# Optimization experiments

Hardware: AMD Instinct MI355X
Metric: run time of the kernel (lower is better)

The kernel has to match this reference:

```python
import jax, jax.numpy as jnp
import numpy as np

S, B, H = 2048, 2, 1024
NH = 16
HD = H // NH
EPS = 1e-5


def _ln(z, w, b):
    m = jnp.mean(z, axis=-1, keepdims=True)
    v = jnp.mean(jnp.square(z - m), axis=-1, keepdims=True)
    return (z - m) * jax.lax.rsqrt(v + EPS) * w + b


def setup_inputs() -> dict:
    key = jax.random.key(0)
    ks = jax.random.split(key, 8)
    std = 0.02
    return {
        "x": jax.random.normal(ks[0], (S, B, H), dtype=jnp.float32),
        "ln1_w": jnp.ones((H,), jnp.float32),
        "ln1_b": jnp.zeros((H,), jnp.float32),
        "w_qkv": jax.random.normal(ks[1], (3 * H, H), jnp.float32) * std,
        "b_qkv": jnp.zeros((3 * H,), jnp.float32),
        "w_proj": jax.random.normal(ks[2], (H, H), jnp.float32) * std,
        "b_proj": jnp.zeros((H,), jnp.float32),
        "ln2_w": jnp.ones((H,), jnp.float32),
        "ln2_b": jnp.zeros((H,), jnp.float32),
        "w_fc1": jax.random.normal(ks[3], (4 * H, H), jnp.float32) * std,
        "b_fc1": jnp.zeros((4 * H,), jnp.float32),
        "w_fc2": jax.random.normal(ks[4], (H, 4 * H), jnp.float32) * std,
        "b_fc2": jnp.zeros((H,), jnp.float32),
    }


def reference(x, ln1_w, ln1_b, w_qkv, b_qkv, w_proj, b_proj,
              ln2_w, ln2_b, w_fc1, b_fc1, w_fc2, b_fc2):
    s, b, h = x.shape
    # --- LayerNormLinear: LN then fused QKV projection ---
    residual = x
    qkv = _ln(x, ln1_w, ln1_b) @ w_qkv.T + b_qkv            # [S, B, 3H]
    # per-head interleaved packing: [S, B, NH, 3*HD] then split on last dim
    qkv = qkv.reshape(s, b, NH, 3 * HD).transpose(1, 2, 0, 3)  # [B, NH, S, 3HD]
    q, k, v = jnp.split(qkv, 3, axis=3)                      # each [B, NH, S, HD]
    # --- naive causal attention with full SxS scores ---
    scores = jnp.einsum("bhsd,bhtd->bhst", q, k) * (HD ** -0.5)
    causal = jnp.triu(jnp.ones((s, s), dtype=bool), k=1)
    scores = jnp.where(causal, -jnp.inf, scores)
    attn = jax.nn.softmax(scores, axis=-1)                   # [B, NH, S, S]
    out = jnp.einsum("bhst,bhtd->bhsd", attn, v)             # [B, NH, S, HD]
    out = out.transpose(0, 2, 1, 3).reshape(b, s, h).transpose(1, 0, 2)  # [S, B, H]
    out = out @ w_proj.T + b_proj
    x = residual + out
    # --- LayerNormMLP: LN -> fc1 -> gelu(tanh) -> fc2, residual ---
    residual = x
    hmid = jax.nn.gelu(_ln(x, ln2_w, ln2_b) @ w_fc1.T + b_fc1, approximate=True)
    x = residual + (hmid @ w_fc2.T + b_fc2)
    return x
```

## Files before the change

### kernel.cpp

```cpp
#include <hip/hip_runtime.h>
#include <math.h>

#define S_LEN 2048
#define B_SZ 2
#define NHEAD 16
#define HDIM 64
#define H_DIM 1024
#define M_ROWS (S_LEN * B_SZ)
#define LN_EPS 1e-5f
#define KSTR 72
#define SCL 0.18033688011112042f

typedef __attribute__((ext_vector_type(4))) float f32x4;
typedef __attribute__((ext_vector_type(8))) short short8;
typedef __attribute__((ext_vector_type(8))) unsigned short u16x8;
typedef __attribute__((ext_vector_type(4))) unsigned short u16x4;
typedef __attribute__((ext_vector_type(2))) unsigned short u16x2;

typedef __attribute__((address_space(3))) unsigned int lds_u32;
typedef const __attribute__((address_space(1))) unsigned int glb_u32;

#define ASM_VMCNT(N) asm volatile("s_waitcnt vmcnt(" #N ")" ::: "memory")

__device__ __forceinline__ float bf2f(unsigned short u) {
    return __uint_as_float(((unsigned int)u) << 16);
}
__device__ __forceinline__ unsigned short f2bf(float f) {
    unsigned int u = __float_as_uint(f);
    return (unsigned short)((u + 0x7fffu + ((u >> 16) & 1u)) >> 16);
}

__global__ __launch_bounds__(256) void cast_all(const float* __restrict__ wqkv,
                                                const float* __restrict__ wproj,
                                                const float* __restrict__ wfc1,
                                                const float* __restrict__ wfc2,
                                                unsigned short* __restrict__ oqkv,
                                                unsigned short* __restrict__ oproj,
                                                unsigned short* __restrict__ ofc1,
                                                unsigned short* __restrict__ ofc2) {
    const int i = blockIdx.x * 256 + threadIdx.x;
    const float* src; unsigned short* dst; int off;
    if (i < 786432)       { src = wqkv;  dst = oqkv;  off = i; }
    else if (i < 1048576) { src = wproj; dst = oproj; off = i - 786432; }
    else if (i < 2097152) { src = wfc1;  dst = ofc1;  off = i - 1048576; }
    else                  { src = wfc2;  dst = ofc2;  off = i - 2097152; }
    f32x4 v = ((const f32x4*)src)[off];
    u16x4 o;
    o.x = f2bf(v.x); o.y = f2bf(v.y); o.z = f2bf(v.z); o.w = f2bf(v.w);
    ((u16x4*)dst)[off] = o;
}

__global__ __launch_bounds__(256) void ln_bf16(const float* __restrict__ x,
                                               const float* __restrict__ w,
                                               const float* __restrict__ b,
                                               unsigned short* __restrict__ y) {
    const int m = blockIdx.x;
    const int tid = threadIdx.x;
    const float* row = x + (size_t)m * H_DIM;

    float4 v = ((const float4*)row)[tid];
    float s  = v.x + v.y + v.z + v.w;
    float ss = v.x * v.x + v.y * v.y + v.z * v.z + v.w * v.w;

    __shared__ float rs[4], rss[4], stats[2];
    const int wave = tid >> 6, lane = tid & 63;
    for (int off = 32; off; off >>= 1) {
        s  += __shfl_down(s, off);
        ss += __shfl_down(ss, off);
    }
    if (lane == 0) { rs[wave] = s; rss[wave] = ss; }
    __syncthreads();
    if (tid == 0) {
        float S = rs[0] + rs[1] + rs[2] + rs[3];
        float SS = rss[0] + rss[1] + rss[2] + rss[3];
        float mean = S * (1.0f / H_DIM);
        float var = SS * (1.0f / H_DIM) - mean * mean;
        stats[0] = mean;
        stats[1] = rsqrtf(var + LN_EPS);
    }
    __syncthreads();
    const float mean = stats[0], inv = stats[1];
    float4 wv = ((const float4*)w)[tid];
    float4 bv = ((const float4*)b)[tid];
    u16x4 o;
    o.x = f2bf((v.x - mean) * inv * wv.x + bv.x);
    o.y = f2bf((v.y - mean) * inv * wv.y + bv.y);
    o.z = f2bf((v.z - mean) * inv * wv.z + bv.z);
    o.w = f2bf((v.w - mean) * inv * wv.w + bv.w);
    ((u16x4*)(y + (size_t)m * H_DIM))[tid] = o;
}

template <int EPI, bool BF_OUT, int TN>
__global__ __launch_bounds__(256) void gemm_mfma(const unsigned short* __restrict__ A,
                                                 const unsigned short* __restrict__ B,
                                                 const float* __restrict__ bias,
                                                 const float* __restrict__ resid,
                                                 void* __restrict__ Cout,
                                                 int M, int N, int K) {
    constexpr int NJ  = TN / 32;
    constexpr int ANI = 4;
    constexpr int BNI = TN / 32;
    constexpr int NBUF = (TN == 128) ? 2 : 3;
    __shared__ __attribute__((aligned(16))) unsigned short As[NBUF][128 * 64];
    __shared__ __attribute__((aligned(16))) unsigned short Bs[NBUF][TN * 64];

    const int tid = threadIdx.x;
    const int wid = tid >> 6;
    const int ln  = tid & 63;
    const int quad = ln >> 4;
    const int mr   = ln & 15;
    const int wm = (wid >> 1) * 64;
    const int wn = (wid & 1) * (TN / 2);

    const int mb = M >> 7;
    const int stripe = mb >> 3;
    const int xcd = blockIdx.x & 7;
    const int local = blockIdx.x >> 3;
    const int m0 = (xcd * stripe + (local % stripe)) << 7;
    const int n0 = (local / stripe) * TN;

    const int lr = ln >> 3, lc = ln & 7;
    const size_t Kb = (size_t)K * 2;
    const char* gA = (const char*)A + (size_t)(m0 + wid * 32 + lr) * Kb
                     + (size_t)((lc << 4) ^ (lr << 4));
    const int bwr = (TN == 128) ? wid * 32 : wid * 16;
    const char* gB = (const char*)B + (size_t)(n0 + bwr + lr) * Kb
                     + (size_t)((lc << 4) ^ (lr << 4));

    auto stage = [&](int kt, int buf) {
        const char* pa = gA + (size_t)kt * 128;
        unsigned int* la = (unsigned int*)&As[buf][0] + wid * (ANI * 256);
#pragma unroll
        for (int i = 0; i < ANI; i++)
            __builtin_amdgcn_global_load_lds((glb_u32*)(pa + (size_t)i * 8 * Kb),
                                             (lds_u32*)(la + i * 256), 16, 0, 0);
        const char* pb = gB + (size_t)kt * 128;
        unsigned int* lb = (unsigned int*)&Bs[buf][0] + wid * (BNI * 256);
#pragma unroll
        for (int i = 0; i < BNI; i++)
            __builtin_amdgcn_global_load_lds((glb_u32*)(pb + (size_t)i * 8 * Kb),
                                             (lds_u32*)(lb + i * 256), 16, 0, 0);
    };

    const f32x4 zero = {0.f, 0.f, 0.f, 0.f};
    f32x4 acc[4][NJ];
#pragma unroll
    for (int i = 0; i < 4; i++)
#pragma unroll
        for (int j = 0; j < NJ; j++) acc[i][j] = zero;

    const int swz = (mr & 7) << 3;
    auto compute = [&](const unsigned short* As_, const unsigned short* Bs_) {
#pragma unroll
        for (int h = 0; h < 2; h++) {
            short8 af[4], bfr[NJ];
#pragma unroll
            for (int i = 0; i < 4; i++)
                af[i] = *(const short8*)(As_ + (wm + i * 16 + mr) * 64
                                             + ((h * 32 + quad * 8) ^ swz));
#pragma unroll
            for (int j = 0; j < NJ; j++)
                bfr[j] = *(const short8*)(Bs_ + (wn + j * 16 + mr) * 64
                                              + ((h * 32 + quad * 8) ^ swz));
#pragma unroll
            for (int i = 0; i < 4; i++)
#pragma unroll
                for (int j = 0; j < NJ; j++)
                    acc[i][j] = __builtin_amdgcn_mfma_f32_16x16x32_bf16(bfr[j], af[i], acc[i][j], 0, 0, 0);
        }
    };

    const int nt = K >> 6;
    stage(0, 0);
    stage(1, 1);
    if (NBUF == 3) stage(2, 2);

    int cb = 0;
    for (int kt = 0; kt < nt; kt++) {
        if (NBUF == 3) {
            if (kt + 2 < nt)      ASM_VMCNT(12);
            else if (kt + 1 < nt) ASM_VMCNT(6);
            else                  ASM_VMCNT(0);
        } else {
            if (kt + 1 < nt)      ASM_VMCNT(8);
            else                  ASM_VMCNT(0);
        }
        __builtin_amdgcn_s_barrier();
        __builtin_amdgcn_sched_barrier(0);
        compute(&As[cb][0], &Bs[cb][0]);
        __builtin_amdgcn_sched_barrier(0);
        __builtin_amdgcn_s_barrier();
        if (kt + NBUF < nt) stage(kt + NBUF, cb);
        cb = (cb + 1 == NBUF) ? 0 : cb + 1;
    }

    f32x4 bias4[NJ];
#pragma unroll
    for (int j = 0; j < NJ; j++)
        bias4[j] = *(const f32x4*)(bias + n0 + wn + j * 16 + quad * 4);

#pragma unroll
    for (int i = 0; i < 4; i++) {
        const int m = m0 + wm + i * 16 + mr;
#pragma unroll
        for (int j = 0; j < NJ; j++) {
            const int nb = n0 + wn + j * 16 + quad * 4;
            f32x4 v = acc[i][j] + bias4[j];
            if (EPI == 1) v += *(const f32x4*)(resid + (size_t)m * N + nb);
            if (EPI == 2) {
#pragma unroll
                for (int r = 0; r < 4; r++) {
                    const float t = v[r];
                    const float u = t + 0.044715f * t * t * t;
                    const float e = exp2f(2.3022112f * u);
                    v[r] = t - t / (e + 1.0f);
                }
            }
            if (BF_OUT) {
                u16x4 pk;
                pk.x = f2bf(v.x); pk.y = f2bf(v.y); pk.z = f2bf(v.z); pk.w = f2bf(v.w);
                *(u16x4*)((unsigned short*)Cout + (size_t)m * N + nb) = pk;
            } else {
                *(f32x4*)((float*)Cout + (size_t)m * N + nb) = v;
            }
        }
    }
}

__global__ __launch_bounds__(256) void attn_mfma(const unsigned short* __restrict__ qkv,
                                                 unsigned short* __restrict__ out) {
    __shared__ __attribute__((aligned(16))) unsigned short Ks[64 * KSTR];
    __shared__ __attribute__((aligned(16))) unsigned short Vs[64 * KSTR];
    __shared__ __attribute__((aligned(16))) unsigned short Ps[64 * KSTR];

    const int tid = threadIdx.x;
    const int wid = tid >> 6;
    const int ln  = tid & 63;
    const int quad = ln >> 4;
    const int mr   = ln & 15;

    const int id = blockIdx.x;
    const int local = id >> 3;
    const int bh = (id & 7) * 4 + (local >> 4);
    const int pa = local & 15;
    const int b  = bh >> 4;
    const int nh = bh & 15;
    const size_t chan = (size_t)nh * 192;

    const int ksr = tid >> 2, ksc = tid & 3;
    const int vt0 = (tid & 31) * 2, vd0 = (tid >> 5) * 8;

    u16x8 kp0, kp1, vp0, vp1;

#pragma unroll
    for (int half = 0; half < 2; half++) {
        const int qt = half ? (31 - pa) : pa;
        const int qb = qt * 64;

        short8 qf0, qf1;
        {
            const int qrow = qb + wid * 16 + mr;
            const unsigned short* gq = qkv + ((size_t)(qrow * 2 + b)) * 3072 + chan + quad * 8;
            qf0 = *(const short8*)gq;
            qf1 = *(const short8*)(gq + 32);
        }

        const f32x4 zero = {0.f, 0.f, 0.f, 0.f};
        f32x4 o[4];
        float ps = 0.f;
#pragma unroll
        for (int d = 0; d < 4; d++) o[d] = zero;

        {
            const unsigned short* gk = qkv + ((size_t)(ksr * 2 + b)) * 3072 + chan + 64 + ksc * 16;
            kp0 = *(const u16x8*)gk;
            kp1 = *(const u16x8*)(gk + 8);
            const unsigned short* gv = qkv + ((size_t)(vt0 * 2 + b)) * 3072 + chan + 128 + vd0;
            vp0 = *(const u16x8*)gv;
            vp1 = *(const u16x8*)(gv + 6144);
        }

        for (int kt = 0; kt <= qt; kt++) {
            __syncthreads();
            *(u16x8*)(Ks + ksr * KSTR + ksc * 16) = kp0;
            *(u16x8*)(Ks + ksr * KSTR + ksc * 16 + 8) = kp1;
#pragma unroll
            for (int j = 0; j < 8; j++) {
                u16x2 pr; pr.x = vp0[j]; pr.y = vp1[j];
                *(u16x2*)(Vs + (vd0 + j) * KSTR + vt0) = pr;
            }
            if (kt < qt) {
                const int nb = (kt + 1) * 64;
                const unsigned short* gk =
                    qkv + ((size_t)((nb + ksr) * 2 + b)) * 3072 + chan + 64 + ksc * 16;
                kp0 = *(const u16x8*)gk;
                kp1 = *(const u16x8*)(gk + 8);
                const unsigned short* gv =
                    qkv + ((size_t)((nb + vt0) * 2 + b)) * 3072 + chan + 128 + vd0;
                vp0 = *(const u16x8*)gv;
                vp1 = *(const u16x8*)(gv + 6144);
            }
            __syncthreads();

            f32x4 sacc[4];
#pragma unroll
            for (int n = 0; n < 4; n++) {
                sacc[n] = zero;
                const unsigned short* kb = Ks + (n * 16 + mr) * KSTR + quad * 8;
                short8 kfr0 = *(const short8*)kb;
                short8 kfr1 = *(const short8*)(kb + 32);
                sacc[n] = __builtin_amdgcn_mfma_f32_16x16x32_bf16(kfr0, qf0, sacc[n], 0, 0, 0);
                sacc[n] = __builtin_amdgcn_mfma_f32_16x16x32_bf16(kfr1, qf1, sacc[n], 0, 0, 0);
            }
            if (kt == qt) {
#pragma unroll
                for (int n = 0; n < 4; n++)
#pragma unroll
                    for (int r = 0; r < 4; r++)
                        if (n * 16 + quad * 4 + r > wid * 16 + mr) sacc[n][r] = -3.0e38f;
            }

            unsigned short* prow = Ps + (wid * 16 + mr) * KSTR + quad * 4;
#pragma unroll
            for (int n = 0; n < 4; n++) {
                u16x4 pk;
#pragma unroll
                for (int r = 0; r < 4; r++) {
                    const float p = exp2f(fminf(sacc[n][r] * SCL, 80.f));
                    ps += p;
                    pk[r] = (unsigned short)(__float_as_uint(p) >> 16);
                }
                *(u16x4*)(prow + n * 16) = pk;
            }

            {
                const unsigned short* pb = Ps + (wid * 16 + mr) * KSTR + quad * 8;
                short8 pa0 = *(const short8*)pb;
                short8 pa1 = *(const short8*)(pb + 32);
#pragma unroll
                for (int d = 0; d < 4; d++) {
                    const unsigned short* vb = Vs + (d * 16 + mr) * KSTR + quad * 8;
                    short8 vf0 = *(const short8*)vb;
                    short8 vf1 = *(const short8*)(vb + 32);
                    o[d] = __builtin_amdgcn_mfma_f32_16x16x32_bf16(vf0, pa0, o[d], 0, 0, 0);
                    o[d] = __builtin_amdgcn_mfma_f32_16x16x32_bf16(vf1, pa1, o[d], 0, 0, 0);
                }
            }
        }

        ps += __shfl_xor(ps, 16);
        ps += __shfl_xor(ps, 32);
        const float inv = 1.0f / ps;
        const int qrow = qb + wid * 16 + mr;
        unsigned short* po = out + ((size_t)(qrow * 2 + b)) * H_DIM + nh * HDIM;
#pragma unroll
        for (int d = 0; d < 4; d++) {
            u16x4 pk;
#pragma unroll
            for (int r = 0; r < 4; r++) pk[r] = f2bf(o[d][r] * inv);
            *(u16x4*)(po + d * 16 + quad * 4) = pk;
        }
    }
}

extern "C" void kernel_launch(void* const* d_in, const int* in_sizes, int n_in,
                              void* d_out, int out_size, void* d_ws, size_t ws_size,
                              hipStream_t stream) {
    const float* x      = (const float*)d_in[0];
    const float* ln1_w  = (const float*)d_in[1];
    const float* ln1_b  = (const float*)d_in[2];
    const float* w_qkv  = (const float*)d_in[3];
    const float* b_qkv  = (const float*)d_in[4];
    const float* w_proj = (const float*)d_in[5];
    const float* b_proj = (const float*)d_in[6];
    const float* ln2_w  = (const float*)d_in[7];
    const float* ln2_b  = (const float*)d_in[8];
    const float* w_fc1  = (const float*)d_in[9];
    const float* b_fc1  = (const float*)d_in[10];
    const float* w_fc2  = (const float*)d_in[11];
    const float* b_fc2  = (const float*)d_in[12];
    float* out = (float*)d_out;

    char* ws = (char*)d_ws;
    unsigned short* wqkv_bf  = (unsigned short*)(ws);
    unsigned short* wproj_bf = (unsigned short*)(ws + ((size_t)6 << 20));
    unsigned short* wfc1_bf  = (unsigned short*)(ws + ((size_t)8 << 20));
    unsigned short* wfc2_bf  = (unsigned short*)(ws + ((size_t)16 << 20));
    unsigned short* ln_buf   = (unsigned short*)(ws + ((size_t)24 << 20));
    unsigned short* qkv_bf   = (unsigned short*)(ws + ((size_t)32 << 20));
    unsigned short* attn_bf  = (unsigned short*)(ws + ((size_t)56 << 20));
    unsigned short* fc1_bf   = (unsigned short*)(ws + ((size_t)32 << 20));

    cast_all<<<12288, 256, 0, stream>>>(w_qkv, w_proj, w_fc1, w_fc2,
                                        wqkv_bf, wproj_bf, wfc1_bf, wfc2_bf);

    ln_bf16<<<M_ROWS, 256, 0, stream>>>(x, ln1_w, ln1_b, ln_buf);
    gemm_mfma<0, true, 128><<<768, 256, 0, stream>>>(
        ln_buf, wqkv_bf, b_qkv, nullptr, qkv_bf, M_ROWS, 3072, 1024);
    attn_mfma<<<512, 256, 0, stream>>>(qkv_bf, attn_bf);
    gemm_mfma<1, false, 64><<<512, 256, 0, stream>>>(
        attn_bf, wproj_bf, b_proj, x, out, M_ROWS, 1024, 1024);
    ln_bf16<<<M_ROWS, 256, 0, stream>>>(out, ln2_w, ln2_b, ln_buf);
    gemm_mfma<2, true, 128><<<1024, 256, 0, stream>>>(
        ln_buf, wfc1_bf, b_fc1, nullptr, fc1_bf, M_ROWS, 4096, 1024);
    gemm_mfma<1, false, 64><<<512, 256, 0, stream>>>(
        fc1_bf, wfc2_bf, b_fc2, out, out, M_ROWS, 1024, 4096);
}
```

Measured before the change: 339.2 us.

## Add 256x256-tile 8-wave GEMM with ping-pong LDS pipeline for QKV and FC1

Adds a new GEMM kernel with 512 threads and 256x256 output tiles. It uses a 4-slot LDS ring filled by direct global-to-LDS loads, XOR swizzling, and split A/B staging interleaved with MFMA phases under barriers and setprio. The QKV and FC1 projections use this kernel instead of the 128-tile one, aiming for more operand reuse and better overlap of loads with MFMA work. The trade-off is fewer blocks (192 and 256, near one per CU) and high register pressure from 32 accumulators per thread, so tail effects and occupancy are at risk.

```diff
diff --git a/kernel.cpp b/kernel.cpp
--- a/kernel.cpp
+++ b/kernel.cpp
@@ -21,6 +21,7 @@
 typedef const __attribute__((address_space(1))) unsigned int glb_u32;
 
 #define ASM_VMCNT(N) asm volatile("s_waitcnt vmcnt(" #N ")" ::: "memory")
+#define ASM_LGKM0()  asm volatile("s_waitcnt lgkmcnt(0)" ::: "memory")
 
 __device__ __forceinline__ float bf2f(unsigned short u) {
     return __uint_as_float(((unsigned int)u) << 16);
@@ -227,6 +228,148 @@
     }
 }
 
+template <int EPI, bool BF_OUT>
+__global__ __launch_bounds__(512, 1) void gemm_8p(const unsigned short* __restrict__ A,
+                                                  const unsigned short* __restrict__ B,
+                                                  const float* __restrict__ bias,
+                                                  const float* __restrict__ resid,
+                                                  void* __restrict__ Cout,
+                                                  int M, int N, int K) {
+    constexpr int SLOT = 256 * 32 * 2;
+    __shared__ __attribute__((aligned(16))) unsigned short Ls[4 * SLOT];
+
+    const int tid = threadIdx.x;
+    const int wid = tid >> 6;
+    const int ln  = tid & 63;
+    const int quad = ln >> 4;
+    const int mr   = ln & 15;
+    const int wr = wid >> 2;
+    const int wc = wid & 3;
+
+    const int nm = M >> 8;
+    const int stripe = nm >> 3;
+    const int xcd = blockIdx.x & 7;
+    const int local = blockIdx.x >> 3;
+    const int m0 = (xcd * stripe + (local % stripe)) << 8;
+    const int n0 = (local / stripe) << 8;
+
+    const int lr2 = ln >> 2, ch = ln & 3;
+    const int sch = ((ch ^ ((lr2 >> 1) & 3)) << 4);
+    const size_t Kb = (size_t)K * 2;
+    const char* gA = (const char*)A + (size_t)(m0 + wid * 32 + lr2) * Kb + sch;
+    const char* gB = (const char*)B + (size_t)(n0 + wid * 32 + lr2) * Kb + sch;
+
+    auto stageA = [&](int kt, int slot) {
+        const char* p = gA + (size_t)kt * 64;
+        unsigned int* l = (unsigned int*)(Ls + slot * SLOT) + (wid * 32) * 16;
+#pragma unroll
+        for (int i = 0; i < 2; i++)
+            __builtin_amdgcn_global_load_lds((glb_u32*)(p + (size_t)(i * 16) * Kb),
+                                             (lds_u32*)(l + i * 256), 16, 0, 0);
+    };
+    auto stageB = [&](int kt, int slot) {
+        const char* p = gB + (size_t)kt * 64;
+        unsigned int* l = (unsigned int*)(Ls + slot * SLOT + 256 * 32) + (wid * 32) * 16;
+#pragma unroll
+        for (int i = 0; i < 2; i++)
+            __builtin_amdgcn_global_load_lds((glb_u32*)(p + (size_t)(i * 16) * Kb),
+                                             (lds_u32*)(l + i * 256), 16, 0, 0);
+    };
+
+    const f32x4 zero = {0.f, 0.f, 0.f, 0.f};
+    f32x4 acc[8][4];
+#pragma unroll
+    for (int i = 0; i < 8; i++)
+#pragma unroll
+        for (int j = 0; j < 4; j++) acc[i][j] = zero;
+
+    const int swzr = ((mr >> 1) & 3) << 4;
+
+    const int nt = K >> 5;
+    stageA(0, 0); stageB(0, 0);
+    stageA(1, 1); stageB(1, 1);
+    ASM_VMCNT(4);
+    __builtin_amdgcn_s_barrier();
+
+    for (int t = 0; t < nt; t++) {
+        const int slot = t & 3;
+        const int s2 = (t + 2) & 3;
+        const unsigned short* sa = Ls + slot * SLOT;
+        const unsigned short* sb = sa + 256 * 32;
+        short8 af[4], bfr[4];
+#pragma unroll
+        for (int i = 0; i < 4; i++)
+            af[i] = *(const short8*)((const char*)sa
+                        + (wr * 128 + i * 16 + mr) * 64 + ((quad << 4) ^ swzr));
+#pragma unroll
+        for (int j = 0; j < 4; j++)
+            bfr[j] = *(const short8*)((const char*)sb
+                        + (wc * 64 + j * 16 + mr) * 64 + ((quad << 4) ^ swzr));
+        if (t + 2 < nt) stageA(t + 2, s2);
+        __builtin_amdgcn_s_barrier();
+        ASM_LGKM0();
+        __builtin_amdgcn_sched_barrier(0);
+        __builtin_amdgcn_s_setprio(1);
+#pragma unroll
+        for (int i = 0; i < 4; i++)
+#pragma unroll
+            for (int j = 0; j < 4; j++)
+                acc[i][j] = __builtin_amdgcn_mfma_f32_16x16x32_bf16(bfr[j], af[i], acc[i][j], 0, 0, 0);
+        __builtin_amdgcn_s_setprio(0);
+        __builtin_amdgcn_s_barrier();
+#pragma unroll
+        for (int i = 0; i < 4; i++)
+            af[i] = *(const short8*)((const char*)sa
+                        + (wr * 128 + 64 + i * 16 + mr) * 64 + ((quad << 4) ^ swzr));
+        if (t + 2 < nt) stageB(t + 2, s2);
+        __builtin_amdgcn_s_barrier();
+        ASM_LGKM0();
+        __builtin_amdgcn_sched_barrier(0);
+        __builtin_amdgcn_s_setprio(1);
+#pragma unroll
+        for (int i = 0; i < 4; i++)
+#pragma unroll
+            for (int j = 0; j < 4; j++)
+                acc[4 + i][j] = __builtin_amdgcn_mfma_f32_16x16x32_bf16(bfr[j], af[i], acc[4 + i][j], 0, 0, 0);
+        __builtin_amdgcn_s_setprio(0);
+        if (t + 2 < nt) ASM_VMCNT(4);
+        else            ASM_VMCNT(0);
+        __builtin_amdgcn_s_barrier();
+    }
+
+    f32x4 bias4[4];
+#pragma unroll
+    for (int j = 0; j < 4; j++)
+        bias4[j] = *(const f32x4*)(bias + n0 + wc * 64 + j * 16 + quad * 4);
+
+#pragma unroll
+    for (int mi = 0; mi < 8; mi++) {
+        const int m = m0 + wr * 128 + mi * 16 + mr;
+#pragma unroll
+        for (int j = 0; j < 4; j++) {
+            const int nb = n0 + wc * 64 + j * 16 + quad * 4;
+            f32x4 v = acc[mi][j] + bias4[j];
+            if (EPI == 1) v += *(const f32x4*)(resid + (size_t)m * N + nb);
+            if (EPI == 2) {
+#pragma unroll
+                for (int r = 0; r < 4; r++) {
+                    const float t = v[r];
+                    const float u = t + 0.044715f * t * t * t;
+                    const float e = exp2f(2.3022112f * u);
+                    v[r] = t - t / (e + 1.0f);
+                }
+            }
+            if (BF_OUT) {
+                u16x4 pk;
+                pk.x = f2bf(v.x); pk.y = f2bf(v.y); pk.z = f2bf(v.z); pk.w = f2bf(v.w);
+                *(u16x4*)((unsigned short*)Cout + (size_t)m * N + nb) = pk;
+            } else {
+                *(f32x4*)((float*)Cout + (size_t)m * N + nb) = v;
+            }
+        }
+    }
+}
+
 __global__ __launch_bounds__(256) void attn_mfma(const unsigned short* __restrict__ qkv,
                                                  unsigned short* __restrict__ out) {
     __shared__ __attribute__((aligned(16))) unsigned short Ks[64 * KSTR];
@@ -395,13 +538,13 @@
                                         wqkv_bf, wproj_bf, wfc1_bf, wfc2_bf);
 
     ln_bf16<<<M_ROWS, 256, 0, stream>>>(x, ln1_w, ln1_b, ln_buf);
-    gemm_mfma<0, true, 128><<<768, 256, 0, stream>>>(
+    gemm_8p<0, true><<<192, 512, 0, stream>>>(
         ln_buf, wqkv_bf, b_qkv, nullptr, qkv_bf, M_ROWS, 3072, 1024);
     attn_mfma<<<512, 256, 0, stream>>>(qkv_bf, attn_bf);
     gemm_mfma<1, false, 64><<<512, 256, 0, stream>>>(
         attn_bf, wproj_bf, b_proj, x, out, M_ROWS, 1024, 1024);
     ln_bf16<<<M_ROWS, 256, 0, stream>>>(out, ln2_w, ln2_b, ln_buf);
-    gemm_mfma<2, true, 128><<<1024, 256, 0, stream>>>(
+    gemm_8p<2, true><<<256, 512, 0, stream>>>(
         ln_buf, wfc1_bf, b_fc1, nullptr, fc1_bf, M_ROWS, 4096, 1024);
     gemm_mfma<1, false, 64><<<512, 256, 0, stream>>>(
         fc1_bf, wfc2_bf, b_fc2, out, out, M_ROWS, 1024, 4096);
```

Result: no change. 339.0 us (-0.1%).
